# Kernel optimization log

Measured on AMD Instinct MI355X. Metric: run time of the kernel, lower is better.

The kernel has to match this reference:

```python
import jax, jax.numpy as jnp
import numpy as np

NUM_CLASSES = 2
THRESHOLD = 0.5


def setup_inputs() -> dict:
    key = jax.random.key(0)
    k1, k2 = jax.random.split(key)
    y_pred = jax.random.uniform(k1, (2, 2, 128, 256, 256), dtype=jnp.float32)
    y_true = jax.random.randint(k2, (2, 128, 256, 256), 0, NUM_CLASSES, dtype=jnp.int32)
    return {"y_pred": y_pred, "y_true": y_true}


def reference(y_pred, y_true):
    C = NUM_CLASSES
    # move channel dim (axis 1) to the end, flatten to [N, C]
    yp = jnp.moveaxis(y_pred, 1, -1).reshape(-1, C)
    yt = y_true.reshape(-1).astype(jnp.int32)
    # has_background=True path: argmax over positive classes (1:), threshold gate
    pos = jnp.argmax(yp[:, 1:], axis=1).astype(jnp.int32) + 1  # [N]
    sel = jnp.take_along_axis(yp, pos[:, None], axis=1)[:, 0]  # prob of chosen positive class
    pred = jnp.where(sel > THRESHOLD, pos, jnp.zeros_like(pos))  # [N] int32
    # single-pass confusion matrix: bincount over y_true*C + y_pred
    idx = yt * C + pred
    cm = jnp.bincount(idx, length=C * C).reshape(C, C).astype(jnp.int32)
    diag = jnp.diagonal(cm)
    fps = cm.sum(axis=0) - diag
    fns = cm.sum(axis=1) - diag
    tps = diag
    tns = cm.sum() - (fps + fns + tps)
    # num_classes == 2 -> scalar stats for class 1
    return (cm, tps[1], fps[1], fns[1], tns[1])
```

## Files before the change

### kernel.cpp

```cpp
#include <hip/hip_runtime.h>

static constexpr long long PER_BATCH = 128LL * 256 * 256;
static constexpr long long N_TOTAL   = 2 * PER_BATCH;
static constexpr long long NV        = N_TOTAL / 4;
static constexpr long long NVB       = PER_BATCH / 4;

static constexpr int       BLOCKS = 2048;
static constexpr int       TPB    = 256;
static constexpr long long T      = (long long)BLOCKS * TPB;

__global__ __launch_bounds__(256) void _cm_count_kernel(
        const float* __restrict__ y_pred,
        const int*   __restrict__ y_true,
        unsigned int* __restrict__ partials) {
    const long long tid = (long long)blockIdx.x * TPB + threadIdx.x;

    const float4* __restrict__ p0 = reinterpret_cast<const float4*>(y_pred + PER_BATCH);
    const float4* __restrict__ p1 = reinterpret_cast<const float4*>(y_pred + 3 * PER_BATCH);
    const int4*   __restrict__ tv = reinterpret_cast<const int4*>(y_true);

    int4   t[8];
    float4 p[8];
    #pragma unroll
    for (int i = 0; i < 8; ++i) t[i] = tv[tid + i * T];
    #pragma unroll
    for (int i = 0; i < 4; ++i) p[i] = p0[tid + i * T];
    #pragma unroll
    for (int i = 0; i < 4; ++i) p[i + 4] = p1[tid + i * T];

    unsigned int ct = 0, cp = 0, cb = 0;
    #pragma unroll
    for (int i = 0; i < 8; ++i) {
        unsigned int t0 = (t[i].x == 1), t1 = (t[i].y == 1), t2 = (t[i].z == 1), t3 = (t[i].w == 1);
        unsigned int q0 = (p[i].x > 0.5f), q1 = (p[i].y > 0.5f), q2 = (p[i].z > 0.5f), q3 = (p[i].w > 0.5f);
        ct += t0 + t1 + t2 + t3;
        cp += q0 + q1 + q2 + q3;
        cb += (t0 & q0) + (t1 & q1) + (t2 & q2) + (t3 & q3);
    }

    #pragma unroll
    for (int off = 32; off > 0; off >>= 1) {
        ct += __shfl_down(ct, off);
        cp += __shfl_down(cp, off);
        cb += __shfl_down(cb, off);
    }

    __shared__ unsigned int s[3][4];
    const int wave = threadIdx.x >> 6;
    if ((threadIdx.x & 63) == 0) { s[0][wave] = ct; s[1][wave] = cp; s[2][wave] = cb; }
    __syncthreads();
    if (threadIdx.x == 0) {
        partials[              blockIdx.x] = s[0][0] + s[0][1] + s[0][2] + s[0][3];
        partials[    BLOCKS + blockIdx.x] = s[1][0] + s[1][1] + s[1][2] + s[1][3];
        partials[2 * BLOCKS + blockIdx.x] = s[2][0] + s[2][1] + s[2][2] + s[2][3];
    }
}

__global__ __launch_bounds__(256) void _cm_finalize_kernel(
        const unsigned int* __restrict__ partials,
        int* __restrict__ out) {
    unsigned int ct = 0, cp = 0, cb = 0;
    #pragma unroll
    for (int i = 0; i < BLOCKS / TPB; ++i) {
        ct += partials[              threadIdx.x + i * TPB];
        cp += partials[    BLOCKS + threadIdx.x + i * TPB];
        cb += partials[2 * BLOCKS + threadIdx.x + i * TPB];
    }
    #pragma unroll
    for (int off = 32; off > 0; off >>= 1) {
        ct += __shfl_down(ct, off);
        cp += __shfl_down(cp, off);
        cb += __shfl_down(cb, off);
    }
    __shared__ unsigned int s[3][4];
    const int wave = threadIdx.x >> 6;
    if ((threadIdx.x & 63) == 0) { s[0][wave] = ct; s[1][wave] = cp; s[2][wave] = cb; }
    __syncthreads();
    if (threadIdx.x == 0) {
        int fct = (int)(s[0][0] + s[0][1] + s[0][2] + s[0][3]);
        int fcp = (int)(s[1][0] + s[1][1] + s[1][2] + s[1][3]);
        int fcb = (int)(s[2][0] + s[2][1] + s[2][2] + s[2][3]);
        int cm11 = fcb;
        int cm10 = fct - fcb;
        int cm01 = fcp - fcb;
        int cm00 = (int)N_TOTAL - fct - fcp + fcb;
        out[0] = cm00; out[1] = cm01;
        out[2] = cm10; out[3] = cm11;
        out[4] = cm11;
        out[5] = cm01;
        out[6] = cm10;
        out[7] = cm00;
    }
}

extern "C" void kernel_launch(void* const* d_in, const int* in_sizes, int n_in,
                              void* d_out, int out_size, void* d_ws, size_t ws_size,
                              hipStream_t stream) {
    const float* y_pred = (const float*)d_in[0];
    const int*   y_true = (const int*)d_in[1];
    unsigned int* partials = (unsigned int*)d_ws;
    int* out = (int*)d_out;

    _cm_count_kernel<<<BLOCKS, TPB, 0, stream>>>(y_pred, y_true, partials);
    _cm_finalize_kernel<<<1, TPB, 0, stream>>>(partials, out);
}
```

Baseline: 213.8 us.

## Fuse finalize into count kernel via atomics and contiguous per-block chunks

Drops the separate finalize kernel. Each block now atomically adds its three counts to a workspace, and the last block to finish, found with an atomic ticket counter, computes the confusion matrix. The access pattern also changes: each block reads one contiguous chunk within a batch instead of a grid-strided layout. This removes one kernel launch but adds a memset launch and contended global atomics.

```diff
diff --git a/kernel.cpp b/kernel.cpp
--- a/kernel.cpp
+++ b/kernel.cpp
@@ -2,35 +2,39 @@
 
 static constexpr long long PER_BATCH = 128LL * 256 * 256;
 static constexpr long long N_TOTAL   = 2 * PER_BATCH;
-static constexpr long long NV        = N_TOTAL / 4;
-static constexpr long long NVB       = PER_BATCH / 4;
 
-static constexpr int       BLOCKS = 2048;
-static constexpr int       TPB    = 256;
-static constexpr long long T      = (long long)BLOCKS * TPB;
+static constexpr int TPB    = 256;
+static constexpr int BLOCKS = 2048;
+static constexpr int BPB    = BLOCKS / 2;
+static constexpr int VEC_PER_BLOCK = (int)(PER_BATCH / 4 / BPB);
+static constexpr int ITERS  = VEC_PER_BLOCK / TPB;
 
-__global__ __launch_bounds__(256) void _cm_count_kernel(
+__global__ __launch_bounds__(TPB) void _cm_count_kernel(
         const float* __restrict__ y_pred,
         const int*   __restrict__ y_true,
-        unsigned int* __restrict__ partials) {
-    const long long tid = (long long)blockIdx.x * TPB + threadIdx.x;
+        unsigned int* __restrict__ ws,
+        int* __restrict__ out) {
+    const int b     = blockIdx.x;
+    const int batch = b >> 10;
+    const int r     = b & (BPB - 1);
+    const int tx    = threadIdx.x;
 
-    const float4* __restrict__ p0 = reinterpret_cast<const float4*>(y_pred + PER_BATCH);
-    const float4* __restrict__ p1 = reinterpret_cast<const float4*>(y_pred + 3 * PER_BATCH);
-    const int4*   __restrict__ tv = reinterpret_cast<const int4*>(y_true);
+    const int4*   __restrict__ tv =
+        reinterpret_cast<const int4*>(y_true + (long long)batch * PER_BATCH);
+    const float4* __restrict__ pv =
+        reinterpret_cast<const float4*>(y_pred + (long long)(2 * batch + 1) * PER_BATCH);
+    const int base = r * VEC_PER_BLOCK + tx;
 
-    int4   t[8];
-    float4 p[8];
+    int4   t[ITERS];
+    float4 p[ITERS];
     #pragma unroll
-    for (int i = 0; i < 8; ++i) t[i] = tv[tid + i * T];
+    for (int i = 0; i < ITERS; ++i) t[i] = tv[base + i * TPB];
     #pragma unroll
-    for (int i = 0; i < 4; ++i) p[i] = p0[tid + i * T];
-    #pragma unroll
-    for (int i = 0; i < 4; ++i) p[i + 4] = p1[tid + i * T];
+    for (int i = 0; i < ITERS; ++i) p[i] = pv[base + i * TPB];
 
     unsigned int ct = 0, cp = 0, cb = 0;
     #pragma unroll
-    for (int i = 0; i < 8; ++i) {
+    for (int i = 0; i < ITERS; ++i) {
         unsigned int t0 = (t[i].x == 1), t1 = (t[i].y == 1), t2 = (t[i].z == 1), t3 = (t[i].w == 1);
         unsigned int q0 = (p[i].x > 0.5f), q1 = (p[i].y > 0.5f), q2 = (p[i].z > 0.5f), q3 = (p[i].w > 0.5f);
         ct += t0 + t1 + t2 + t3;
@@ -46,40 +50,28 @@
     }
 
     __shared__ unsigned int s[3][4];
-    const int wave = threadIdx.x >> 6;
-    if ((threadIdx.x & 63) == 0) { s[0][wave] = ct; s[1][wave] = cp; s[2][wave] = cb; }
+    __shared__ int lastFlag;
+    const int wave = tx >> 6;
+    if ((tx & 63) == 0) { s[0][wave] = ct; s[1][wave] = cp; s[2][wave] = cb; }
     __syncthreads();
-    if (threadIdx.x == 0) {
-        partials[              blockIdx.x] = s[0][0] + s[0][1] + s[0][2] + s[0][3];
-        partials[    BLOCKS + blockIdx.x] = s[1][0] + s[1][1] + s[1][2] + s[1][3];
-        partials[2 * BLOCKS + blockIdx.x] = s[2][0] + s[2][1] + s[2][2] + s[2][3];
+
+    if (tx == 0) {
+        unsigned int bct = s[0][0] + s[0][1] + s[0][2] + s[0][3];
+        unsigned int bcp = s[1][0] + s[1][1] + s[1][2] + s[1][3];
+        unsigned int bcb = s[2][0] + s[2][1] + s[2][2] + s[2][3];
+        atomicAdd(&ws[0], bct);
+        atomicAdd(&ws[1], bcp);
+        atomicAdd(&ws[2], bcb);
+        __threadfence();
+        lastFlag = (atomicAdd(&ws[3], 1u) == (unsigned)(BLOCKS - 1));
     }
-}
+    __syncthreads();
 
-__global__ __launch_bounds__(256) void _cm_finalize_kernel(
-        const unsigned int* __restrict__ partials,
-        int* __restrict__ out) {
-    unsigned int ct = 0, cp = 0, cb = 0;
-    #pragma unroll
-    for (int i = 0; i < BLOCKS / TPB; ++i) {
-        ct += partials[              threadIdx.x + i * TPB];
-        cp += partials[    BLOCKS + threadIdx.x + i * TPB];
-        cb += partials[2 * BLOCKS + threadIdx.x + i * TPB];
-    }
-    #pragma unroll
-    for (int off = 32; off > 0; off >>= 1) {
-        ct += __shfl_down(ct, off);
-        cp += __shfl_down(cp, off);
-        cb += __shfl_down(cb, off);
-    }
-    __shared__ unsigned int s[3][4];
-    const int wave = threadIdx.x >> 6;
-    if ((threadIdx.x & 63) == 0) { s[0][wave] = ct; s[1][wave] = cp; s[2][wave] = cb; }
-    __syncthreads();
-    if (threadIdx.x == 0) {
-        int fct = (int)(s[0][0] + s[0][1] + s[0][2] + s[0][3]);
-        int fcp = (int)(s[1][0] + s[1][1] + s[1][2] + s[1][3]);
-        int fcb = (int)(s[2][0] + s[2][1] + s[2][2] + s[2][3]);
+    if (tx == 0 && lastFlag) {
+        __threadfence();
+        int fct = (int)atomicAdd(&ws[0], 0u);
+        int fcp = (int)atomicAdd(&ws[1], 0u);
+        int fcb = (int)atomicAdd(&ws[2], 0u);
         int cm11 = fcb;
         int cm10 = fct - fcb;
         int cm01 = fcp - fcb;
@@ -98,9 +90,9 @@
                               hipStream_t stream) {
     const float* y_pred = (const float*)d_in[0];
     const int*   y_true = (const int*)d_in[1];
-    unsigned int* partials = (unsigned int*)d_ws;
+    unsigned int* ws = (unsigned int*)d_ws;
     int* out = (int*)d_out;
 
-    _cm_count_kernel<<<BLOCKS, TPB, 0, stream>>>(y_pred, y_true, partials);
-    _cm_finalize_kernel<<<1, TPB, 0, stream>>>(partials, out);
+    hipMemsetAsync(ws, 0, 4 * sizeof(unsigned int), stream);
+    _cm_count_kernel<<<BLOCKS, TPB, 0, stream>>>(y_pred, y_true, ws, out);
 }
```

Result: slower. 314.0 us (+46.9%).

## Split counting kernel into separate prediction-mask and label passes

Applied to the files above, without the earlier changes.

Splits the single fused counting kernel into two kernels. The first reads y_pred, packs the threshold results into a 64-bit bitmask per thread and counts positives. The second reads y_true together with the mask and counts true positives and label positives. The likely aim is to shorten each kernel's load stream and lower register pressure. In exchange it adds a mask write and read through global memory (about 4 MB), one extra kernel launch, and removes overlap between the two input streams.

```diff
diff --git a/kernel.cpp b/kernel.cpp
--- a/kernel.cpp
+++ b/kernel.cpp
@@ -2,83 +2,116 @@
 
 static constexpr long long PER_BATCH = 128LL * 256 * 256;
 static constexpr long long N_TOTAL   = 2 * PER_BATCH;
-static constexpr long long NV        = N_TOTAL / 4;
 static constexpr long long NVB       = PER_BATCH / 4;
 
 static constexpr int       BLOCKS = 2048;
 static constexpr int       TPB    = 256;
 static constexpr long long T      = (long long)BLOCKS * TPB;
 
-__global__ __launch_bounds__(256) void _cm_count_kernel(
+static constexpr size_t MASK_U64 = (size_t)T;
+
+__device__ __forceinline__ void block_reduce_store(unsigned int v,
+                                                   unsigned int* __restrict__ dst) {
+    #pragma unroll
+    for (int off = 32; off > 0; off >>= 1) v += __shfl_down(v, off);
+    __shared__ unsigned int s[4];
+    const int wave = threadIdx.x >> 6;
+    if ((threadIdx.x & 63) == 0) s[wave] = v;
+    __syncthreads();
+    if (threadIdx.x == 0) dst[blockIdx.x] = s[0] + s[1] + s[2] + s[3];
+}
+
+__global__ __launch_bounds__(TPB) void _cm_pred_kernel(
         const float* __restrict__ y_pred,
-        const int*   __restrict__ y_true,
-        unsigned int* __restrict__ partials) {
+        unsigned long long* __restrict__ mask64,
+        unsigned int* __restrict__ cp_part) {
     const long long tid = (long long)blockIdx.x * TPB + threadIdx.x;
-
     const float4* __restrict__ p0 = reinterpret_cast<const float4*>(y_pred + PER_BATCH);
     const float4* __restrict__ p1 = reinterpret_cast<const float4*>(y_pred + 3 * PER_BATCH);
-    const int4*   __restrict__ tv = reinterpret_cast<const int4*>(y_true);
 
-    int4   t[8];
     float4 p[8];
-    #pragma unroll
-    for (int i = 0; i < 8; ++i) t[i] = tv[tid + i * T];
     #pragma unroll
     for (int i = 0; i < 4; ++i) p[i] = p0[tid + i * T];
     #pragma unroll
     for (int i = 0; i < 4; ++i) p[i + 4] = p1[tid + i * T];
 
-    unsigned int ct = 0, cp = 0, cb = 0;
+    unsigned long long m = 0;
     #pragma unroll
     for (int i = 0; i < 8; ++i) {
-        unsigned int t0 = (t[i].x == 1), t1 = (t[i].y == 1), t2 = (t[i].z == 1), t3 = (t[i].w == 1);
-        unsigned int q0 = (p[i].x > 0.5f), q1 = (p[i].y > 0.5f), q2 = (p[i].z > 0.5f), q3 = (p[i].w > 0.5f);
+        unsigned int b = (unsigned int)(p[i].x > 0.5f)
+                       | ((unsigned int)(p[i].y > 0.5f) << 1)
+                       | ((unsigned int)(p[i].z > 0.5f) << 2)
+                       | ((unsigned int)(p[i].w > 0.5f) << 3);
+        m |= (unsigned long long)b << (8 * i);
+    }
+    mask64[tid] = m;
+    block_reduce_store((unsigned int)__popcll(m), cp_part);
+}
+
+__global__ __launch_bounds__(TPB) void _cm_true_kernel(
+        const int* __restrict__ y_true,
+        const unsigned long long* __restrict__ mask64,
+        unsigned int* __restrict__ ct_part,
+        unsigned int* __restrict__ cb_part) {
+    const long long tid = (long long)blockIdx.x * TPB + threadIdx.x;
+    const int4* __restrict__ tv = reinterpret_cast<const int4*>(y_true);
+
+    int4 t[8];
+    #pragma unroll
+    for (int i = 0; i < 8; ++i) t[i] = tv[tid + i * T];
+    const unsigned long long m = mask64[tid];
+
+    unsigned int ct = 0, cb = 0;
+    #pragma unroll
+    for (int i = 0; i < 8; ++i) {
+        unsigned int t0 = (t[i].x == 1), t1 = (t[i].y == 1),
+                     t2 = (t[i].z == 1), t3 = (t[i].w == 1);
+        unsigned int bi = (unsigned int)(m >> (8 * i)) & 0xFu;
         ct += t0 + t1 + t2 + t3;
-        cp += q0 + q1 + q2 + q3;
-        cb += (t0 & q0) + (t1 & q1) + (t2 & q2) + (t3 & q3);
+        cb += (t0 & (bi & 1u)) + (t1 & ((bi >> 1) & 1u))
+            + (t2 & ((bi >> 2) & 1u)) + (t3 & ((bi >> 3) & 1u));
     }
 
     #pragma unroll
     for (int off = 32; off > 0; off >>= 1) {
         ct += __shfl_down(ct, off);
-        cp += __shfl_down(cp, off);
         cb += __shfl_down(cb, off);
     }
-
-    __shared__ unsigned int s[3][4];
+    __shared__ unsigned int s[2][4];
     const int wave = threadIdx.x >> 6;
-    if ((threadIdx.x & 63) == 0) { s[0][wave] = ct; s[1][wave] = cp; s[2][wave] = cb; }
+    if ((threadIdx.x & 63) == 0) { s[0][wave] = ct; s[1][wave] = cb; }
     __syncthreads();
     if (threadIdx.x == 0) {
-        partials[              blockIdx.x] = s[0][0] + s[0][1] + s[0][2] + s[0][3];
-        partials[    BLOCKS + blockIdx.x] = s[1][0] + s[1][1] + s[1][2] + s[1][3];
-        partials[2 * BLOCKS + blockIdx.x] = s[2][0] + s[2][1] + s[2][2] + s[2][3];
+        ct_part[blockIdx.x] = s[0][0] + s[0][1] + s[0][2] + s[0][3];
+        cb_part[blockIdx.x] = s[1][0] + s[1][1] + s[1][2] + s[1][3];
     }
 }
 
-__global__ __launch_bounds__(256) void _cm_finalize_kernel(
-        const unsigned int* __restrict__ partials,
+__global__ __launch_bounds__(TPB) void _cm_finalize_kernel(
+        const unsigned int* __restrict__ cp_part,
+        const unsigned int* __restrict__ ct_part,
+        const unsigned int* __restrict__ cb_part,
         int* __restrict__ out) {
-    unsigned int ct = 0, cp = 0, cb = 0;
+    unsigned int cp = 0, ct = 0, cb = 0;
     #pragma unroll
     for (int i = 0; i < BLOCKS / TPB; ++i) {
-        ct += partials[              threadIdx.x + i * TPB];
-        cp += partials[    BLOCKS + threadIdx.x + i * TPB];
-        cb += partials[2 * BLOCKS + threadIdx.x + i * TPB];
+        cp += cp_part[threadIdx.x + i * TPB];
+        ct += ct_part[threadIdx.x + i * TPB];
+        cb += cb_part[threadIdx.x + i * TPB];
     }
     #pragma unroll
     for (int off = 32; off > 0; off >>= 1) {
+        cp += __shfl_down(cp, off);
         ct += __shfl_down(ct, off);
-        cp += __shfl_down(cp, off);
         cb += __shfl_down(cb, off);
     }
     __shared__ unsigned int s[3][4];
     const int wave = threadIdx.x >> 6;
-    if ((threadIdx.x & 63) == 0) { s[0][wave] = ct; s[1][wave] = cp; s[2][wave] = cb; }
+    if ((threadIdx.x & 63) == 0) { s[0][wave] = cp; s[1][wave] = ct; s[2][wave] = cb; }
     __syncthreads();
     if (threadIdx.x == 0) {
-        int fct = (int)(s[0][0] + s[0][1] + s[0][2] + s[0][3]);
-        int fcp = (int)(s[1][0] + s[1][1] + s[1][2] + s[1][3]);
+        int fcp = (int)(s[0][0] + s[0][1] + s[0][2] + s[0][3]);
+        int fct = (int)(s[1][0] + s[1][1] + s[1][2] + s[1][3]);
         int fcb = (int)(s[2][0] + s[2][1] + s[2][2] + s[2][3]);
         int cm11 = fcb;
         int cm10 = fct - fcb;
@@ -98,9 +131,13 @@
                               hipStream_t stream) {
     const float* y_pred = (const float*)d_in[0];
     const int*   y_true = (const int*)d_in[1];
-    unsigned int* partials = (unsigned int*)d_ws;
+    unsigned long long* mask64 = (unsigned long long*)d_ws;
+    unsigned int* cp_part = (unsigned int*)((char*)d_ws + MASK_U64 * 8);
+    unsigned int* ct_part = cp_part + BLOCKS;
+    unsigned int* cb_part = ct_part + BLOCKS;
     int* out = (int*)d_out;
 
-    _cm_count_kernel<<<BLOCKS, TPB, 0, stream>>>(y_pred, y_true, partials);
-    _cm_finalize_kernel<<<1, TPB, 0, stream>>>(partials, out);
+    _cm_pred_kernel<<<BLOCKS, TPB, 0, stream>>>(y_pred, mask64, cp_part);
+    _cm_true_kernel<<<BLOCKS, TPB, 0, stream>>>(y_true, mask64, ct_part, cb_part);
+    _cm_finalize_kernel<<<1, TPB, 0, stream>>>(cp_part, ct_part, cb_part, out);
 }
```

Result: no change. 217.4 us (+1.7%).
